# Performance work log

Measured on AMD Instinct MI355X. Metric: run time of the kernel, lower is better.

## Reference

```python
import jax, jax.numpy as jnp
import numpy as np

# dims
B, T, N, D = 4, 256, 64, 512
H, DH = 8, 64            # n_head, d_head; H*DH == D
DF = 4 * D               # SwiGLU hidden
EPS = 1e-6


def rmsnorm(x, w):
    return x * jax.lax.rsqrt(jnp.mean(x * x, axis=-1, keepdims=True) + EPS) * w


def phi(x):
    # positive feature map for kernelized (linear) attention ('SMReg' assumed elu+1 style)
    return jax.nn.elu(x) + 1.0


def heads(x):
    return x.reshape(*x.shape[:-1], H, DH)


def lin_att(Xq, Xkv, wq, wk, wv, wo):
    # low-rank high-order linear attention: kernelized attention applied
    # independently along each tensor mode (time T, entities N), averaged.
    q = phi(heads(Xq @ wq))   # [B,T,N,H,DH]
    k = phi(heads(Xkv @ wk))
    v = heads(Xkv @ wv)
    # mode 1 (time): attend over T, batch over (B,N)
    kv_t = jnp.einsum('btnhk,btnhv->bnhkv', k, v)          # [B,N,H,DH,DH]
    ks_t = k.sum(axis=1)                                   # [B,N,H,DH]
    den_t = jnp.einsum('btnhk,bnhk->btnh', q, ks_t) + EPS
    out_t = jnp.einsum('btnhk,bnhkv->btnhv', q, kv_t) / den_t[..., None]
    # mode 2 (entities): attend over N, batch over (B,T)
    kv_n = jnp.einsum('btnhk,btnhv->bthkv', k, v)
    ks_n = k.sum(axis=2)
    den_n = jnp.einsum('btnhk,bthk->btnh', q, ks_n) + EPS
    out_n = jnp.einsum('btnhk,bthkv->btnhv', q, kv_n) / den_n[..., None]
    out = 0.5 * (out_t + out_n)
    return out.reshape(*Xq.shape[:-1], H * DH) @ wo


def swiglu(x, w1, w2, w3):
    return (jax.nn.silu(x @ w1) * (x @ w3)) @ w2


def setup_inputs() -> dict:
    key = jax.random.key(0)
    ks = jax.random.split(key, 20)
    s = 0.02
    inp = {
        'X': jax.random.normal(ks[0], (B, T, N, D), jnp.float32),
        'Z': jax.random.normal(ks[1], (B, T, N, D), jnp.float32),
        'n1': jnp.ones((D,), jnp.float32),
        'n2': jnp.ones((D,), jnp.float32),
        'n3': jnp.ones((D,), jnp.float32),
        'nz': jnp.ones((D,), jnp.float32),
        'a_wq': jax.random.normal(ks[2], (D, H * DH), jnp.float32) * s,
        'a_wk': jax.random.normal(ks[3], (D, H * DH), jnp.float32) * s,
        'a_wv': jax.random.normal(ks[4], (D, H * DH), jnp.float32) * s,
        'a_wo': jax.random.normal(ks[5], (H * DH, D), jnp.float32) * s,
        'c_wq': jax.random.normal(ks[6], (D, H * DH), jnp.float32) * s,
        'c_wk': jax.random.normal(ks[7], (D, H * DH), jnp.float32) * s,
        'c_wv': jax.random.normal(ks[8], (D, H * DH), jnp.float32) * s,
        'c_wo': jax.random.normal(ks[9], (H * DH, D), jnp.float32) * s,
        'f_w1': jax.random.normal(ks[10], (D, DF), jnp.float32) * s,
        'f_w2': jax.random.normal(ks[11], (DF, D), jnp.float32) * s,
        'f_w3': jax.random.normal(ks[12], (D, DF), jnp.float32) * s,
    }
    return inp


def reference(X, Z, n1, n2, n3, nz, a_wq, a_wk, a_wv, a_wo,
              c_wq, c_wk, c_wv, c_wo, f_w1, f_w2, f_w3):
    # h = X + SelfAtt(norm1(X))
    xn = rmsnorm(X, n1)
    h = X + lin_att(xn, xn, a_wq, a_wk, a_wv, a_wo)
    # h = h + CrossAtt(norm3(h), normz(Z))
    h = h + lin_att(rmsnorm(h, n3), rmsnorm(Z, nz), c_wq, c_wk, c_wv, c_wo)
    # out = h + SwiGLU(norm2(h))   (dropout p=0 -> identity)
    return h + swiglu(rmsnorm(h, n2), f_w1, f_w2, f_w3)
```

## Files before the change

### kernel.cpp

```cpp
#include <hip/hip_runtime.h>

typedef short s16x8 __attribute__((ext_vector_type(8)));
typedef float f32x4 __attribute__((ext_vector_type(4)));
typedef unsigned short u16;
typedef unsigned int u32;

__device__ __forceinline__ float bf2f(u16 u) {
  union { unsigned int i; float f; } v; v.i = ((unsigned int)u) << 16; return v.f;
}
__device__ __forceinline__ u16 f2bf(float f) {
  union { float f; unsigned int i; } v; v.f = f;
  unsigned int r = v.i + 0x7fffu + ((v.i >> 16) & 1u);
  return (u16)(r >> 16);
}

__device__ __forceinline__ void gload16(const u16* g, u16* l) {
  __builtin_amdgcn_global_load_lds(
      (const __attribute__((address_space(1))) u32*)g,
      (__attribute__((address_space(3))) u32*)l, 16, 0, 0);
}

template<int KDIM, int NDIM>
__launch_bounds__(256)
__global__ void wprep(const float* __restrict__ in, u16* __restrict__ out) {
  __shared__ float t[64][65];
  const int tid = threadIdx.x;
  const int nb = NDIM / 64;
  const int tk0 = (blockIdx.x / nb) * 64;
  const int tn0 = (blockIdx.x % nb) * 64;
#pragma unroll
  for (int i = 0; i < 16; i++) {
    int idx = i * 256 + tid;
    int r = idx >> 6, c = idx & 63;
    t[r][c] = in[(long)(tk0 + r) * NDIM + (tn0 + c)];
  }
  __syncthreads();
#pragma unroll
  for (int i = 0; i < 16; i++) {
    int idx = i * 256 + tid;
    int nn = idx >> 6, kk = idx & 63;
    out[(long)(tn0 + nn) * KDIM + (tk0 + kk)] = f2bf(t[kk][nn]);
  }
}

__launch_bounds__(256)
__global__ void rmsnorm_f32(const float* __restrict__ x, const float* __restrict__ w,
                            u16* __restrict__ out) {
  const long row = (long)blockIdx.x * 4 + (threadIdx.x >> 6);
  const int lane = threadIdx.x & 63;
  const float* xr = x + row * 512 + lane * 8;
  float4 v0 = *(const float4*)xr;
  float4 v1 = *(const float4*)(xr + 4);
  float ss = v0.x*v0.x + v0.y*v0.y + v0.z*v0.z + v0.w*v0.w
           + v1.x*v1.x + v1.y*v1.y + v1.z*v1.z + v1.w*v1.w;
#pragma unroll
  for (int o = 1; o < 64; o <<= 1) ss += __shfl_xor(ss, o);
  float sc = rsqrtf(ss * (1.0f / 512.0f) + 1e-6f);
  const float* wp = w + lane * 8;
  float4 w0 = *(const float4*)wp;
  float4 w1 = *(const float4*)(wp + 4);
  union { u16 u[8]; uint4 v; } o;
  o.u[0] = f2bf(v0.x * sc * w0.x);
  o.u[1] = f2bf(v0.y * sc * w0.y);
  o.u[2] = f2bf(v0.z * sc * w0.z);
  o.u[3] = f2bf(v0.w * sc * w0.w);
  o.u[4] = f2bf(v1.x * sc * w1.x);
  o.u[5] = f2bf(v1.y * sc * w1.y);
  o.u[6] = f2bf(v1.z * sc * w1.z);
  o.u[7] = f2bf(v1.w * sc * w1.w);
  *(uint4*)(out + row * 512 + lane * 8) = o.v;
}

__launch_bounds__(256)
__global__ void rmsnorm_bf16(const u16* __restrict__ x, const float* __restrict__ w,
                             u16* __restrict__ out) {
  const long row = (long)blockIdx.x * 4 + (threadIdx.x >> 6);
  const int lane = threadIdx.x & 63;
  uint4 u = *(const uint4*)(x + row * 512 + lane * 8);
  const u16* us = (const u16*)&u;
  float f[8];
  float ss = 0.f;
#pragma unroll
  for (int j = 0; j < 8; j++) { f[j] = bf2f(us[j]); ss += f[j] * f[j]; }
#pragma unroll
  for (int o = 1; o < 64; o <<= 1) ss += __shfl_xor(ss, o);
  float sc = rsqrtf(ss * (1.0f / 512.0f) + 1e-6f);
  const float* wp = w + lane * 8;
  union { u16 u[8]; uint4 v; } o;
#pragma unroll
  for (int j = 0; j < 8; j++) o.u[j] = f2bf(f[j] * sc * wp[j]);
  *(uint4*)(out + row * 512 + lane * 8) = o.v;
}

enum { EPI_BF16 = 0, EPI_PHI = 1, EPI_RESX = 2, EPI_RESH = 3, EPI_SILUMUL = 4, EPI_OUTF = 5 };

template<int KD, int EPI>
__launch_bounds__(256)
__global__ void gemm2(const u16* __restrict__ A, const u16* __restrict__ Bt,
                      void* __restrict__ Cout, const void* __restrict__ aux,
                      int Ns) {
  __shared__ u16 As[2][128][64];
  __shared__ u16 Bs[2][128][64];
  const int tid = threadIdx.x;
  const int lane = tid & 63;
  const int wv = tid >> 6;
  const int nwgx = gridDim.x;
  int L = blockIdx.y * nwgx + blockIdx.x;
  const int cpx = (nwgx * gridDim.y) >> 3;
  L = (L & 7) * cpx + (L >> 3);
  const long m0 = (long)(L / nwgx) * 128;
  const long n0 = (long)(L % nwgx) * 128;

  const int wr = (wv >> 1) * 64;
  const int wc = (wv & 1) * 64;
  const int fr = lane & 15;
  const int fkb = (lane >> 4) * 8;

  const u16* Ag = A + (m0 + (lane >> 3)) * KD + (lane & 7) * 8;
  const u16* Bg = Bt + (n0 + (lane >> 3)) * KD + (lane & 7) * 8;

  f32x4 acc[4][4] = {};

  auto STAGE = [&](int b, int k0) {
#pragma unroll
    for (int i = 0; i < 4; i++) {
      const int r8 = (i * 4 + wv) * 8;
      gload16(Ag + (long)r8 * KD + k0, &As[b][r8][0]);
      gload16(Bg + (long)r8 * KD + k0, &Bs[b][r8][0]);
    }
  };
  auto COMPUTE = [&](int b) {
#pragma unroll
    for (int ks = 0; ks < 2; ks++) {
      s16x8 af[4], bf[4];
#pragma unroll
      for (int i = 0; i < 4; i++) af[i] = *(const s16x8*)&As[b][wr + i * 16 + fr][ks * 32 + fkb];
#pragma unroll
      for (int j = 0; j < 4; j++) bf[j] = *(const s16x8*)&Bs[b][wc + j * 16 + fr][ks * 32 + fkb];
#pragma unroll
      for (int i = 0; i < 4; i++)
#pragma unroll
        for (int j = 0; j < 4; j++)
          acc[i][j] = __builtin_amdgcn_mfma_f32_16x16x32_bf16(af[i], bf[j], acc[i][j], 0, 0, 0);
    }
  };

  constexpr int NT = KD / 64;
  STAGE(0, 0);
  __syncthreads();
#pragma unroll 1
  for (int kt = 0; kt < NT - 2; kt += 2) {
    STAGE(1, (kt + 1) * 64);
    COMPUTE(0);
    __syncthreads();
    STAGE(0, (kt + 2) * 64);
    COMPUTE(1);
    __syncthreads();
  }
  STAGE(1, (NT - 1) * 64);
  COMPUTE(0);
  __syncthreads();
  COMPUTE(1);

  const int col = lane & 15;
  const int rb = (lane >> 4) * 4;
#pragma unroll
  for (int i = 0; i < 4; i++) {
#pragma unroll
    for (int r = 0; r < 4; r++) {
      long m = m0 + wr + i * 16 + rb + r;
#pragma unroll
      for (int j = 0; j < 4; j++) {
        long n = n0 + wc + j * 16 + col;
        long off = m * Ns + n;
        float v = acc[i][j][r];
        if constexpr (EPI == EPI_BF16) {
          ((u16*)Cout)[off] = f2bf(v);
        } else if constexpr (EPI == EPI_PHI) {
          float p = v > 0.f ? v + 1.f : __expf(v);
          ((u16*)Cout)[off] = f2bf(p);
        } else if constexpr (EPI == EPI_RESX) {
          ((u16*)Cout)[off] = f2bf(((const float*)aux)[off] + v);
        } else if constexpr (EPI == EPI_RESH) {
          ((u16*)Cout)[off] = f2bf(bf2f(((const u16*)aux)[off]) + v);
        } else if constexpr (EPI == EPI_SILUMUL) {
          float t = bf2f(((const u16*)aux)[off]);
          float s = t / (1.f + __expf(-t));
          ((u16*)Cout)[off] = f2bf(s * v);
        } else {
          ((float*)Cout)[off] = bf2f(((const u16*)aux)[off]) + v;
        }
      }
    }
  }
}

__launch_bounds__(256)
__global__ void att_mode1(const u16* __restrict__ q, const u16* __restrict__ k,
                          const u16* __restrict__ v, u16* __restrict__ attc) {
  __shared__ u16 Ks[128][72];
  __shared__ u16 Vs[128][72];
  __shared__ u16 KVT[64][72];
  __shared__ float ksump[4][64];
  __shared__ float ksum_s[64];
  __shared__ float dinv[256];
  const int tid = threadIdx.x;
  const int lane = tid & 63;
  const int w = tid >> 6;
  const int bnh = blockIdx.x;
  const int h = bnh & 7;
  const int bn = bnh >> 3;
  const int n = bn & 63;
  const int b = bn >> 6;
  const long base = ((long)b * 16384 + n) * 512 + h * 64;
  const int fr = lane & 15;
  const int fk = (lane >> 4) * 8;
  const int sdk = tid & 63, sqq = tid >> 6;

  f32x4 acc[4] = {};
  float ks_acc = 0.f;

  for (int half = 0; half < 2; half++) {
    __syncthreads();
#pragma unroll
    for (int rep = 0; rep < 4; rep++) {
      int idx = rep * 256 + tid;
      int tl = idx >> 3, c8 = idx & 7;
      long go = base + (long)(half * 128 + tl) * 32768 + c8 * 8;
      *(uint4*)&Ks[tl][c8 * 8] = *(const uint4*)(k + go);
      *(uint4*)&Vs[tl][c8 * 8] = *(const uint4*)(v + go);
    }
    __syncthreads();
#pragma unroll
    for (int i = 0; i < 32; i++) ks_acc += bf2f(Ks[sqq * 32 + i][sdk]);
#pragma unroll
    for (int ks = 0; ks < 4; ks++) {
      s16x8 af, bfr[4];
#pragma unroll
      for (int e = 0; e < 8; e++) af[e] = (short)Vs[ks * 32 + fk + e][w * 16 + fr];
#pragma unroll
      for (int j = 0; j < 4; j++)
#pragma unroll
        for (int e = 0; e < 8; e++) bfr[j][e] = (short)Ks[ks * 32 + fk + e][j * 16 + fr];
#pragma unroll
      for (int j = 0; j < 4; j++)
        acc[j] = __builtin_amdgcn_mfma_f32_16x16x32_bf16(af, bfr[j], acc[j], 0, 0, 0);
    }
  }
  ksump[sqq][sdk] = ks_acc;
  __syncthreads();
  {
    const int colL = lane & 15, rb = (lane >> 4) * 4;
#pragma unroll
    for (int j = 0; j < 4; j++)
#pragma unroll
      for (int r = 0; r < 4; r++)
        KVT[w * 16 + rb + r][j * 16 + colL] = f2bf(acc[j][r]);
  }
  if (tid < 64) ksum_s[tid] = ksump[0][tid] + ksump[1][tid] + ksump[2][tid] + ksump[3][tid];
  __syncthreads();
  {
    const u16* qp = q + base + (long)tid * 32768;
    float d = 0.f;
#pragma unroll
    for (int c8 = 0; c8 < 8; c8++) {
      uint4 u = ((const uint4*)qp)[c8];
      const u16* us = (const u16*)&u;
#pragma unroll
      for (int e = 0; e < 8; e++) d += bf2f(us[e]) * ksum_s[c8 * 8 + e];
    }
    dinv[tid] = 0.5f / (d + 1e-6f);
  }
  f32x4 acc2[4][4] = {};
#pragma unroll
  for (int ks = 0; ks < 2; ks++) {
    s16x8 aq[4], bk[4];
#pragma unroll
    for (int i = 0; i < 4; i++)
      aq[i] = *(const s16x8*)(q + base + (long)(w * 64 + i * 16 + fr) * 32768 + ks * 32 + fk);
#pragma unroll
    for (int j = 0; j < 4; j++)
      bk[j] = *(const s16x8*)&KVT[j * 16 + fr][ks * 32 + fk];
#pragma unroll
    for (int i = 0; i < 4; i++)
#pragma unroll
      for (int j = 0; j < 4; j++)
        acc2[i][j] = __builtin_amdgcn_mfma_f32_16x16x32_bf16(aq[i], bk[j], acc2[i][j], 0, 0, 0);
  }
  __syncthreads();
  const int colL = lane & 15, rb = (lane >> 4) * 4;
#pragma unroll
  for (int i = 0; i < 4; i++)
#pragma unroll
    for (int r = 0; r < 4; r++) {
      int t = w * 64 + i * 16 + rb + r;
      float inv = dinv[t];
#pragma unroll
      for (int j = 0; j < 4; j++)
        attc[base + (long)t * 32768 + j * 16 + colL] = f2bf(acc2[i][j][r] * inv);
    }
}

__launch_bounds__(256)
__global__ void att_mode2(const u16* __restrict__ q, const u16* __restrict__ k,
                          const u16* __restrict__ v, u16* __restrict__ attc) {
  __shared__ u16 Ks[64][72];
  __shared__ u16 Vs[64][72];
  __shared__ u16 KVT[64][72];
  __shared__ float ksump[4][64];
  __shared__ float ksum_s[64];
  __shared__ float dinv[64];
  const int tid = threadIdx.x;
  const int lane = tid & 63;
  const int w = tid >> 6;
  const int bth = blockIdx.x;
  const int h = bth & 7;
  const long bt = bth >> 3;
  const long base = bt * 32768 + h * 64;
  const int fr = lane & 15;
  const int fk = (lane >> 4) * 8;
  const int sdk = tid & 63, sqq = tid >> 6;

#pragma unroll
  for (int rep = 0; rep < 2; rep++) {
    int idx = rep * 256 + tid;
    int nl = idx >> 3, c8 = idx & 7;
    long go = base + (long)nl * 512 + c8 * 8;
    *(uint4*)&Ks[nl][c8 * 8] = *(const uint4*)(k + go);
    *(uint4*)&Vs[nl][c8 * 8] = *(const uint4*)(v + go);
  }
  __syncthreads();
  {
    float s = 0.f;
#pragma unroll
    for (int i = 0; i < 16; i++) s += bf2f(Ks[sqq * 16 + i][sdk]);
    ksump[sqq][sdk] = s;
  }
  f32x4 acc[4] = {};
#pragma unroll
  for (int ks = 0; ks < 2; ks++) {
    s16x8 af, bfr[4];
#pragma unroll
    for (int e = 0; e < 8; e++) af[e] = (short)Vs[ks * 32 + fk + e][w * 16 + fr];
#pragma unroll
    for (int j = 0; j < 4; j++)
#pragma unroll
      for (int e = 0; e < 8; e++) bfr[j][e] = (short)Ks[ks * 32 + fk + e][j * 16 + fr];
#pragma unroll
    for (int j = 0; j < 4; j++)
      acc[j] = __builtin_amdgcn_mfma_f32_16x16x32_bf16(af, bfr[j], acc[j], 0, 0, 0);
  }
  __syncthreads();
  {
    const int colL = lane & 15, rb = (lane >> 4) * 4;
#pragma unroll
    for (int j = 0; j < 4; j++)
#pragma unroll
      for (int r = 0; r < 4; r++)
        KVT[w * 16 + rb + r][j * 16 + colL] = f2bf(acc[j][r]);
  }
  if (tid < 64) ksum_s[tid] = ksump[0][tid] + ksump[1][tid] + ksump[2][tid] + ksump[3][tid];
  __syncthreads();
  if (tid < 64) {
    const u16* qp = q + base + (long)tid * 512;
    float d = 0.f;
#pragma unroll
    for (int c8 = 0; c8 < 8; c8++) {
      uint4 u = ((const uint4*)qp)[c8];
      const u16* us = (const u16*)&u;
#pragma unroll
      for (int e = 0; e < 8; e++) d += bf2f(us[e]) * ksum_s[c8 * 8 + e];
    }
    dinv[tid] = 0.5f / (d + 1e-6f);
  }
  f32x4 acc2[4] = {};
#pragma unroll
  for (int ks = 0; ks < 2; ks++) {
    s16x8 aq, bk[4];
    aq = *(const s16x8*)(q + base + (long)(w * 16 + fr) * 512 + ks * 32 + fk);
#pragma unroll
    for (int j = 0; j < 4; j++)
      bk[j] = *(const s16x8*)&KVT[j * 16 + fr][ks * 32 + fk];
#pragma unroll
    for (int j = 0; j < 4; j++)
      acc2[j] = __builtin_amdgcn_mfma_f32_16x16x32_bf16(aq, bk[j], acc2[j], 0, 0, 0);
  }
  __syncthreads();
  const int colL = lane & 15, rb = (lane >> 4) * 4;
#pragma unroll
  for (int r = 0; r < 4; r++) {
    int nr = w * 16 + rb + r;
    float inv = dinv[nr];
#pragma unroll
    for (int j = 0; j < 4; j++) {
      long o = base + (long)nr * 512 + j * 16 + colL;
      attc[o] = f2bf(bf2f(attc[o]) + acc2[j][r] * inv);
    }
  }
}

extern "C" void kernel_launch(void* const* d_in, const int* in_sizes, int n_in,
                              void* d_out, int out_size, void* d_ws, size_t ws_size,
                              hipStream_t stream) {
  const float* X    = (const float*)d_in[0];
  const float* Z    = (const float*)d_in[1];
  const float* n1   = (const float*)d_in[2];
  const float* n2   = (const float*)d_in[3];
  const float* n3   = (const float*)d_in[4];
  const float* nz   = (const float*)d_in[5];
  const float* a_wq = (const float*)d_in[6];
  const float* a_wk = (const float*)d_in[7];
  const float* a_wv = (const float*)d_in[8];
  const float* a_wo = (const float*)d_in[9];
  const float* c_wq = (const float*)d_in[10];
  const float* c_wk = (const float*)d_in[11];
  const float* c_wv = (const float*)d_in[12];
  const float* c_wo = (const float*)d_in[13];
  const float* f_w1 = (const float*)d_in[14];
  const float* f_w2 = (const float*)d_in[15];
  const float* f_w3 = (const float*)d_in[16];
  float* out = (float*)d_out;
  (void)ws_size; (void)in_sizes; (void)n_in; (void)out_size;

  char* p = (char*)d_ws;
  size_t off = 0;
  auto take = [&](size_t bytes) -> char* {
    char* r = p + off;
    off += (bytes + 255) & ~(size_t)255;
    return r;
  };
  u16* w_aq = (u16*)take(512 * 512 * 2);
  u16* w_ak = (u16*)take(512 * 512 * 2);
  u16* w_av = (u16*)take(512 * 512 * 2);
  u16* w_ao = (u16*)take(512 * 512 * 2);
  u16* w_cq = (u16*)take(512 * 512 * 2);
  u16* w_ck = (u16*)take(512 * 512 * 2);
  u16* w_cv = (u16*)take(512 * 512 * 2);
  u16* w_co = (u16*)take(512 * 512 * 2);
  u16* w_f1 = (u16*)take(2048 * 512 * 2);
  u16* w_f3 = (u16*)take(2048 * 512 * 2);
  u16* w_f2 = (u16*)take(512 * 2048 * 2);
  u16* xn   = (u16*)take((size_t)65536 * 512 * 2);
  u16* hbuf = (u16*)take((size_t)65536 * 512 * 2);
  u16* qbuf = (u16*)take((size_t)65536 * 512 * 2);
  u16* kbuf = (u16*)d_out;
  u16* vbuf = (u16*)d_out + (size_t)65536 * 512;
  u16* attc = xn;
  u16* tslot = qbuf;

  dim3 b256(256);
  dim3 gP(4, 512);
  dim3 gU(16, 128);
  dim3 gD(4, 128);

  wprep<512, 512><<<64, b256, 0, stream>>>(a_wq, w_aq);
  wprep<512, 512><<<64, b256, 0, stream>>>(a_wk, w_ak);
  wprep<512, 512><<<64, b256, 0, stream>>>(a_wv, w_av);
  wprep<512, 512><<<64, b256, 0, stream>>>(a_wo, w_ao);
  wprep<512, 512><<<64, b256, 0, stream>>>(c_wq, w_cq);
  wprep<512, 512><<<64, b256, 0, stream>>>(c_wk, w_ck);
  wprep<512, 512><<<64, b256, 0, stream>>>(c_wv, w_cv);
  wprep<512, 512><<<64, b256, 0, stream>>>(c_wo, w_co);
  wprep<512, 2048><<<256, b256, 0, stream>>>(f_w1, w_f1);
  wprep<512, 2048><<<256, b256, 0, stream>>>(f_w3, w_f3);
  wprep<2048, 512><<<256, b256, 0, stream>>>(f_w2, w_f2);

  rmsnorm_f32<<<16384, b256, 0, stream>>>(X, n1, xn);
  gemm2<512, EPI_PHI><<<gP, b256, 0, stream>>>(xn, w_aq, qbuf, nullptr, 512);
  gemm2<512, EPI_PHI><<<gP, b256, 0, stream>>>(xn, w_ak, kbuf, nullptr, 512);
  gemm2<512, EPI_BF16><<<gP, b256, 0, stream>>>(xn, w_av, vbuf, nullptr, 512);
  att_mode1<<<2048, b256, 0, stream>>>(qbuf, kbuf, vbuf, attc);
  att_mode2<<<8192, b256, 0, stream>>>(qbuf, kbuf, vbuf, attc);
  gemm2<512, EPI_RESX><<<gP, b256, 0, stream>>>(attc, w_ao, hbuf, X, 512);

  rmsnorm_bf16<<<16384, b256, 0, stream>>>(hbuf, n3, xn);
  gemm2<512, EPI_PHI><<<gP, b256, 0, stream>>>(xn, w_cq, qbuf, nullptr, 512);
  rmsnorm_f32<<<16384, b256, 0, stream>>>(Z, nz, xn);
  gemm2<512, EPI_PHI><<<gP, b256, 0, stream>>>(xn, w_ck, kbuf, nullptr, 512);
  gemm2<512, EPI_BF16><<<gP, b256, 0, stream>>>(xn, w_cv, vbuf, nullptr, 512);
  att_mode1<<<2048, b256, 0, stream>>>(qbuf, kbuf, vbuf, attc);
  att_mode2<<<8192, b256, 0, stream>>>(qbuf, kbuf, vbuf, attc);
  gemm2<512, EPI_RESH><<<gP, b256, 0, stream>>>(attc, w_co, hbuf, hbuf, 512);

  rmsnorm_bf16<<<16384, b256, 0, stream>>>(hbuf, n2, xn);
  const int CH = 16384;
  for (int c = 0; c < 4; c++) {
    const size_t ro = (size_t)c * CH * 512;
    const size_t rf = (size_t)c * CH * 2048;
    (void)rf;
    gemm2<512, EPI_BF16><<<gU, b256, 0, stream>>>(xn + ro * 4 / 4, w_f1, tslot, nullptr, 2048);
    gemm2<512, EPI_SILUMUL><<<gU, b256, 0, stream>>>(xn + ro, w_f3, tslot, tslot, 2048);
    gemm2<2048, EPI_OUTF><<<gD, b256, 0, stream>>>(tslot, w_f2, out + ro, hbuf + ro, 512);
  }
}
```

Baseline: 1.714 ms.

## Replace 128x128 GEMM with 256x256-tile 512-thread kernel using swizzled LDS

Replaces the 128x128-tile, 256-thread GEMM with a 256x256-tile, 512-thread kernel in which each wave computes a 128x64 sub-tile. The LDS layout gets an XOR swizzle to avoid bank conflicts, and the double-buffered loop now uses explicit vmcnt waits so the next tile's loads overlap compute. Larger tiles raise operand reuse and cut global traffic per FLOP. In exchange, register pressure (128 accumulator floats) and LDS use (128KB) rise, and there are fewer workgroups per launch.

```diff
diff --git a/kernel.cpp b/kernel.cpp
--- a/kernel.cpp
+++ b/kernel.cpp
@@ -95,50 +95,55 @@
 enum { EPI_BF16 = 0, EPI_PHI = 1, EPI_RESX = 2, EPI_RESH = 3, EPI_SILUMUL = 4, EPI_OUTF = 5 };
 
 template<int KD, int EPI>
-__launch_bounds__(256)
-__global__ void gemm2(const u16* __restrict__ A, const u16* __restrict__ Bt,
-                      void* __restrict__ Cout, const void* __restrict__ aux,
-                      int Ns) {
-  __shared__ u16 As[2][128][64];
-  __shared__ u16 Bs[2][128][64];
+__launch_bounds__(512)
+__global__ void gemm256(const u16* __restrict__ A, const u16* __restrict__ Bt,
+                        void* __restrict__ Cout, const void* __restrict__ aux,
+                        int Ns) {
+  __shared__ u16 As[2][256][64];
+  __shared__ u16 Bs[2][256][64];
   const int tid = threadIdx.x;
   const int lane = tid & 63;
-  const int wv = tid >> 6;
-  const int nwgx = gridDim.x;
-  int L = blockIdx.y * nwgx + blockIdx.x;
-  const int cpx = (nwgx * gridDim.y) >> 3;
+  const int wid = tid >> 6;
+  const int gx = gridDim.x;
+  int L = blockIdx.y * gx + blockIdx.x;
+  const int cpx = (gx * gridDim.y) >> 3;
   L = (L & 7) * cpx + (L >> 3);
-  const long m0 = (long)(L / nwgx) * 128;
-  const long n0 = (long)(L % nwgx) * 128;
-
-  const int wr = (wv >> 1) * 64;
-  const int wc = (wv & 1) * 64;
+  const long m0 = (long)(L / gx) * 256;
+  const long n0 = (long)(L % gx) * 256;
+
+  const int wrbase = (wid >> 2) * 128;
+  const int wcbase = (wid & 3) * 64;
   const int fr = lane & 15;
-  const int fkb = (lane >> 4) * 8;
-
-  const u16* Ag = A + (m0 + (lane >> 3)) * KD + (lane & 7) * 8;
-  const u16* Bg = Bt + (n0 + (lane >> 3)) * KD + (lane & 7) * 8;
-
-  f32x4 acc[4][4] = {};
-
-  auto STAGE = [&](int b, int k0) {
-#pragma unroll
-    for (int i = 0; i < 4; i++) {
-      const int r8 = (i * 4 + wv) * 8;
-      gload16(Ag + (long)r8 * KD + k0, &As[b][r8][0]);
-      gload16(Bg + (long)r8 * KD + k0, &Bs[b][r8][0]);
+  const int frq = lane >> 4;
+
+  const int rA0 = wid * 8 + (lane >> 3);
+  const int sg8 = (((lane & 7) ^ ((lane >> 3) & 7))) * 8;
+  const u16* Ag = A + (m0 + rA0) * KD + sg8;
+  const u16* Bg = Bt + (n0 + rA0) * KD + sg8;
+  u16* Alds = &As[0][0][0] + wid * 512;
+  u16* Blds = &Bs[0][0][0] + wid * 512;
+
+  f32x4 acc[8][4] = {};
+
+  auto STAGE = [&](int b, int kt) {
+    const long k0 = (long)kt * 64;
+#pragma unroll
+    for (int j = 0; j < 4; j++) {
+      gload16(Ag + (long)(j * 64) * KD + k0, Alds + b * 16384 + j * 4096);
+      gload16(Bg + (long)(j * 64) * KD + k0, Blds + b * 16384 + j * 4096);
     }
   };
   auto COMPUTE = [&](int b) {
 #pragma unroll
     for (int ks = 0; ks < 2; ks++) {
-      s16x8 af[4], bf[4];
-#pragma unroll
-      for (int i = 0; i < 4; i++) af[i] = *(const s16x8*)&As[b][wr + i * 16 + fr][ks * 32 + fkb];
-#pragma unroll
-      for (int j = 0; j < 4; j++) bf[j] = *(const s16x8*)&Bs[b][wc + j * 16 + fr][ks * 32 + fkb];
-#pragma unroll
-      for (int i = 0; i < 4; i++)
+      const int slot = ((ks * 4 + frq) ^ (fr & 7)) * 8;
+      s16x8 af[8], bf[4];
+#pragma unroll
+      for (int i = 0; i < 8; i++) af[i] = *(const s16x8*)&As[b][wrbase + i * 16 + fr][slot];
+#pragma unroll
+      for (int j = 0; j < 4; j++) bf[j] = *(const s16x8*)&Bs[b][wcbase + j * 16 + fr][slot];
+#pragma unroll
+      for (int i = 0; i < 8; i++)
 #pragma unroll
         for (int j = 0; j < 4; j++)
           acc[i][j] = __builtin_amdgcn_mfma_f32_16x16x32_bf16(af[i], bf[j], acc[i][j], 0, 0, 0);
@@ -147,31 +152,30 @@
 
   constexpr int NT = KD / 64;
   STAGE(0, 0);
-  __syncthreads();
 #pragma unroll 1
-  for (int kt = 0; kt < NT - 2; kt += 2) {
-    STAGE(1, (kt + 1) * 64);
-    COMPUTE(0);
-    __syncthreads();
-    STAGE(0, (kt + 2) * 64);
-    COMPUTE(1);
-    __syncthreads();
-  }
-  STAGE(1, (NT - 1) * 64);
-  COMPUTE(0);
-  __syncthreads();
-  COMPUTE(1);
+  for (int t = 0; t < NT; ++t) {
+    if (t + 1 < NT) {
+      STAGE((t + 1) & 1, t + 1);
+      asm volatile("s_waitcnt vmcnt(8)" ::: "memory");
+    } else {
+      asm volatile("s_waitcnt vmcnt(0)" ::: "memory");
+    }
+    __builtin_amdgcn_s_barrier();
+    COMPUTE(t & 1);
+    asm volatile("s_waitcnt lgkmcnt(0)" ::: "memory");
+    __builtin_amdgcn_s_barrier();
+  }
 
   const int col = lane & 15;
-  const int rb = (lane >> 4) * 4;
-#pragma unroll
-  for (int i = 0; i < 4; i++) {
+  const int rb = frq * 4;
+#pragma unroll
+  for (int i = 0; i < 8; i++) {
 #pragma unroll
     for (int r = 0; r < 4; r++) {
-      long m = m0 + wr + i * 16 + rb + r;
+      long m = m0 + wrbase + i * 16 + rb + r;
 #pragma unroll
       for (int j = 0; j < 4; j++) {
-        long n = n0 + wc + j * 16 + col;
+        long n = n0 + wcbase + j * 16 + col;
         long off = m * Ns + n;
         float v = acc[i][j][r];
         if constexpr (EPI == EPI_BF16) {
@@ -184,8 +188,8 @@
         } else if constexpr (EPI == EPI_RESH) {
           ((u16*)Cout)[off] = f2bf(bf2f(((const u16*)aux)[off]) + v);
         } else if constexpr (EPI == EPI_SILUMUL) {
-          float t = bf2f(((const u16*)aux)[off]);
-          float s = t / (1.f + __expf(-t));
+          float t2 = bf2f(((const u16*)aux)[off]);
+          float s = t2 / (1.f + __expf(-t2));
           ((u16*)Cout)[off] = f2bf(s * v);
         } else {
           ((float*)Cout)[off] = bf2f(((const u16*)aux)[off]) + v;
@@ -449,9 +453,10 @@
   u16* tslot = qbuf;
 
   dim3 b256(256);
-  dim3 gP(4, 512);
-  dim3 gU(16, 128);
-  dim3 gD(4, 128);
+  dim3 b512(512);
+  dim3 gP(2, 256);
+  dim3 gU(8, 64);
+  dim3 gD(2, 64);
 
   wprep<512, 512><<<64, b256, 0, stream>>>(a_wq, w_aq);
   wprep<512, 512><<<64, b256, 0, stream>>>(a_wk, w_ak);
@@ -466,30 +471,28 @@
   wprep<2048, 512><<<256, b256, 0, stream>>>(f_w2, w_f2);
 
   rmsnorm_f32<<<16384, b256, 0, stream>>>(X, n1, xn);
-  gemm2<512, EPI_PHI><<<gP, b256, 0, stream>>>(xn, w_aq, qbuf, nullptr, 512);
-  gemm2<512, EPI_PHI><<<gP, b256, 0, stream>>>(xn, w_ak, kbuf, nullptr, 512);
-  gemm2<512, EPI_BF16><<<gP, b256, 0, stream>>>(xn, w_av, vbuf, nullptr, 512);
+  gemm256<512, EPI_PHI><<<gP, b512, 0, stream>>>(xn, w_aq, qbuf, nullptr, 512);
+  gemm256<512, EPI_PHI><<<gP, b512, 0, stream>>>(xn, w_ak, kbuf, nullptr, 512);
+  gemm256<512, EPI_BF16><<<gP, b512, 0, stream>>>(xn, w_av, vbuf, nullptr, 512);
   att_mode1<<<2048, b256, 0, stream>>>(qbuf, kbuf, vbuf, attc);
   att_mode2<<<8192, b256, 0, stream>>>(qbuf, kbuf, vbuf, attc);
-  gemm2<512, EPI_RESX><<<gP, b256, 0, stream>>>(attc, w_ao, hbuf, X, 512);
+  gemm256<512, EPI_RESX><<<gP, b512, 0, stream>>>(attc, w_ao, hbuf, X, 512);
 
   rmsnorm_bf16<<<16384, b256, 0, stream>>>(hbuf, n3, xn);
-  gemm2<512, EPI_PHI><<<gP, b256, 0, stream>>>(xn, w_cq, qbuf, nullptr, 512);
+  gemm256<512, EPI_PHI><<<gP, b512, 0, stream>>>(xn, w_cq, qbuf, nullptr, 512);
   rmsnorm_f32<<<16384, b256, 0, stream>>>(Z, nz, xn);
-  gemm2<512, EPI_PHI><<<gP, b256, 0, stream>>>(xn, w_ck, kbuf, nullptr, 512);
-  gemm2<512, EPI_BF16><<<gP, b256, 0, stream>>>(xn, w_cv, vbuf, nullptr, 512);
+  gemm256<512, EPI_PHI><<<gP, b512, 0, stream>>>(xn, w_ck, kbuf, nullptr, 512);
+  gemm256<512, EPI_BF16><<<gP, b512, 0, stream>>>(xn, w_cv, vbuf, nullptr, 512);
   att_mode1<<<2048, b256, 0, stream>>>(qbuf, kbuf, vbuf, attc);
   att_mode2<<<8192, b256, 0, stream>>>(qbuf, kbuf, vbuf, attc);
-  gemm2<512, EPI_RESH><<<gP, b256, 0, stream>>>(attc, w_co, hbuf, hbuf, 512);
+  gemm256<512, EPI_RESH><<<gP, b512, 0, stream>>>(attc, w_co, hbuf, hbuf, 512);
 
   rmsnorm_bf16<<<16384, b256, 0, stream>>>(hbuf, n2, xn);
   const int CH = 16384;
   for (int c = 0; c < 4; c++) {
     const size_t ro = (size_t)c * CH * 512;
-    const size_t rf = (size_t)c * CH * 2048;
-    (void)rf;
-    gemm2<512, EPI_BF16><<<gU, b256, 0, stream>>>(xn + ro * 4 / 4, w_f1, tslot, nullptr, 2048);
-    gemm2<512, EPI_SILUMUL><<<gU, b256, 0, stream>>>(xn + ro, w_f3, tslot, tslot, 2048);
-    gemm2<2048, EPI_OUTF><<<gD, b256, 0, stream>>>(tslot, w_f2, out + ro, hbuf + ro, 512);
-  }
-}
+    gemm256<512, EPI_BF16><<<gU, b512, 0, stream>>>(xn + ro, w_f1, tslot, nullptr, 2048);
+    gemm256<512, EPI_SILUMUL><<<gU, b512, 0, stream>>>(xn + ro, w_f3, tslot, tslot, 2048);
+    gemm256<2048, EPI_OUTF><<<gD, b512, 0, stream>>>(tslot, w_f2, out + ro, hbuf + ro, 512);
+  }
+}
```

Result: faster. 1.565 ms (-8.7%).
